# Performance work log

Measured on AMD Instinct MI355X. Metric: run time of the kernel, lower is better.

Reference implementation:

```python
import itertools
import jax
import jax.numpy as jnp
import numpy as np

FRAME_H, FRAME_W = 480, 640
HFOV = 79
CAM_H_CM = 88.0
NUM_SEM = 16
MAP_SIZE_CM, RES = 4800, 5
VR = 100
BEEN_CLOSE_CM = 200
GDS = 2
DU = 4
CAT_THR, EXP_THR, MAP_THR = 5.0, 1.0, 1.0
MIN_D_CM, MAX_D_CM = 50.0, 350.0
MIN_OBS_H_CM = 25
DIL_ITER, DIL_SIZE = 1, 3

NON_SEM = 4
LOCAL = MAP_SIZE_CM // GDS // RES
GLOBAL = MAP_SIZE_CM // RES
MAX_VH = int(360 / RES)
MIN_VH = int(-40 / RES)
ZB = MAX_VH - MIN_VH
MIN_Z = int(MIN_OBS_H_CM / RES - MIN_VH)
MAX_Z = int((CAM_H_CM + 1) / RES - MIN_VH)
XC = (FRAME_W - 1) / 2.0
ZC = (FRAME_H - 1) / 2.0
FOCAL = (FRAME_W / 2.0) / np.tan(np.deg2rad(HFOV / 2.0))
DEG = 57.29577951308232
B, T = 2, 4
C_MAP = NON_SEM + NUM_SEM

GPOSE0 = jnp.array([24.0, 24.0, 0.0], jnp.float32)
ORIG0 = jnp.array([12.0, 12.0, 0.0], jnp.float32)
LPOSE0 = GPOSE0 - ORIG0
LMB0 = jnp.array([240, 720, 240, 720], jnp.int32)

_XS = np.arange(FRAME_W, dtype=np.float32)[::DU]
_ZS = np.arange(FRAME_H - 1, -1, -1, dtype=np.float32)[::DU]


def point_cloud(depth):
    d = depth[:, ::DU, ::DU]
    valid = (d > MIN_D_CM) & (d < MAX_D_CM)
    X = (_XS[None, None, :] - XC) * d / FOCAL
    Z = (_ZS[None, :, None] - ZC) * d / FOCAL
    pts = jnp.stack([X, d, Z], -1).reshape(d.shape[0], -1, 3)
    return pts, valid.reshape(d.shape[0], -1)


def avg_pool(x, k):
    b, c, h, w = x.shape
    return x.reshape(b, c, h // k, k, w // k, k).mean((3, 5))


def splat(feat, coords):
    bs, fc, n = feat.shape
    dims = (VR, VR, ZB)
    G = VR * VR * ZB
    pos = [coords[:, d] * dims[d] / 2.0 + dims[d] / 2.0 for d in range(3)]
    fl = [jnp.floor(p) for p in pos]
    out = jnp.zeros((fc, bs * G), feat.dtype)
    offs = (jnp.arange(bs) * G)[:, None]
    for corner in itertools.product((0.0, 1.0), repeat=3):
        idx = jnp.zeros_like(pos[0])
        w = jnp.ones_like(pos[0])
        for d in range(3):
            p = fl[d] + corner[d]
            safe = ((p > 0) & (p < dims[d])).astype(feat.dtype)
            w = w * (1.0 - jnp.abs(pos[d] - p)) * safe
            idx = idx * dims[d] + p * safe
        flat = (idx.astype(jnp.int32) + offs).reshape(-1)
        vals = (feat * w[:, None, :]).transpose(1, 0, 2).reshape(fc, -1)
        out = out.at[:, flat].add(vals)
    out = jnp.round(out)
    return out.reshape(fc, bs, VR, VR, ZB).transpose(1, 0, 2, 3, 4)


def affine_grid(theta, h, w):
    ys = jnp.linspace(-1.0, 1.0, h)
    xs = jnp.linspace(-1.0, 1.0, w)
    gy, gx = jnp.meshgrid(ys, xs, indexing="ij")
    base = jnp.stack([gx, gy, jnp.ones_like(gx)], -1)
    return jnp.einsum("bij,hwj->bhwi", theta, base)


def _sample_one(im, grid):
    c, h, w = im.shape
    x = (grid[..., 0] + 1.0) * (w - 1) / 2.0
    y = (grid[..., 1] + 1.0) * (h - 1) / 2.0
    x0 = jnp.floor(x)
    y0 = jnp.floor(y)
    out = jnp.zeros((c,) + x.shape, im.dtype)
    for dx, dy in ((0, 0), (1, 0), (0, 1), (1, 1)):
        xi = x0 + dx
        yi = y0 + dy
        wgt = (1.0 - jnp.abs(x - xi)) * (1.0 - jnp.abs(y - yi))
        ok = (xi >= 0) & (xi <= w - 1) & (yi >= 0) & (yi <= h - 1)
        xi_c = jnp.clip(xi, 0, w - 1).astype(jnp.int32)
        yi_c = jnp.clip(yi, 0, h - 1).astype(jnp.int32)
        out = out + im[:, yi_c, xi_c] * (wgt * ok)[None]
    return out


grid_sample = jax.vmap(_sample_one)


def get_new_pose(pose, rel):
    s = jnp.sin(pose[:, 2] / DEG)
    c = jnp.cos(pose[:, 2] / DEG)
    x = pose[:, 0] + rel[:, 0] * c - rel[:, 1] * s
    y = pose[:, 1] + rel[:, 0] * s + rel[:, 1] * c
    o = pose[:, 2] + rel[:, 2] * DEG
    o = jnp.fmod(o - 180.0, 360.0) + 180.0
    o = jnp.fmod(o + 180.0, 360.0) - 180.0
    return jnp.stack([x, y, o], 1)


def update_local(obs, pdelta, prev_map, prev_pose):
    bs = obs.shape[0]
    pts, valid = point_cloud(obs[:, 3])
    pts = pts.at[..., 2].add(CAM_H_CM)
    pts = pts.at[..., 0].add(VR * RES / 2.0)
    cx = (pts[..., 0] / RES - VR // 2) / VR * 2.0
    cy = (pts[..., 1] / RES - VR // 2) / VR * 2.0
    cz = (pts[..., 2] / RES - (MAX_VH + MIN_VH) // 2) / ZB * 2.0
    coords = jnp.stack([cx, cy, cz], 1)
    coords = jnp.where(valid[:, None, :], coords, 2.0)
    sem = avg_pool(obs[:, 4:], DU).reshape(bs, NUM_SEM, -1)
    feat = jnp.concatenate([jnp.ones_like(sem[:, :1]), sem], 1)
    vox = splat(feat, coords)
    agent_h = vox[..., MIN_Z:MAX_Z].sum(-1)
    all_h = vox.sum(-1)
    fp_map = jnp.clip(agent_h[:, :1] / MAP_THR, 0.0, 1.0)
    fp_exp = jnp.clip(all_h[:, :1] / EXP_THR, 0.0, 1.0)
    sem_pred = jnp.clip(agent_h[:, 1:] / CAT_THR, 0.0, 1.0)
    x1 = LOCAL // 2 - VR // 2
    y1 = LOCAL // 2
    av = jnp.zeros((bs, C_MAP, LOCAL, LOCAL), obs.dtype)
    av = av.at[:, 0:1, y1:y1 + VR, x1:x1 + VR].set(fp_map)
    av = av.at[:, 1:2, y1:y1 + VR, x1:x1 + VR].set(fp_exp)
    av = av.at[:, NON_SEM:, y1:y1 + VR, x1:x1 + VR].set(sem_pred)
    pose = get_new_pose(prev_pose, pdelta)
    half = LOCAL // 2
    stx = -(pose[:, 0] * 100.0 / RES - half) / half
    sty = -(pose[:, 1] * 100.0 / RES - half) / half
    th = (90.0 - pose[:, 2]) * (np.pi / 180.0)
    ct, snt = jnp.cos(th), jnp.sin(th)
    zr, on = jnp.zeros_like(ct), jnp.ones_like(ct)
    th1 = jnp.stack([jnp.stack([ct, -snt, zr], -1), jnp.stack([snt, ct, zr], -1)], 1)
    th2 = jnp.stack([jnp.stack([on, zr, stx], -1), jnp.stack([zr, on, sty], -1)], 1)
    rotated = grid_sample(av, affine_grid(th1, LOCAL, LOCAL))
    translated = grid_sample(rotated, affine_grid(th2, LOCAL, LOCAL))
    cur = jnp.maximum(prev_map, translated)
    obst = cur[:, 0:1]
    kern = jnp.ones((1, 1, DIL_SIZE, DIL_SIZE), cur.dtype)
    for _ in range(DIL_ITER):
        obst = (jax.lax.conv(obst, kern, (1, 1), "SAME") > 0.5).astype(cur.dtype)
    cur = cur.at[:, 0].set(obst[:, 0])
    xg = (pose[:, 0] * 100.0 / RES).astype(jnp.int32)
    yg = (pose[:, 1] * 100.0 / RES).astype(jnp.int32)
    rr = jnp.arange(LOCAL)
    drow = rr[None, :, None] - yg[:, None, None]
    dcol = rr[None, None, :] - xg[:, None, None]
    sq = ((jnp.abs(drow) <= 2) & (jnp.abs(dcol) <= 2)).astype(cur.dtype)
    cur = cur.at[:, 2].set(sq)
    rad = BEEN_CLOSE_CM // RES
    disk = ((drow * drow + dcol * dcol) <= rad * rad).astype(cur.dtype)
    cur = cur.at[:, 3].set(jnp.maximum(cur[:, 3], disk))
    return cur, pose


def update_global_env(lmap, gmap, lpose, gpose, lmb, orig, updg):
    gpose_n = lpose + orig
    gmap_n = jax.lax.dynamic_update_slice(gmap, lmap, (0, lmb[0], lmb[2]))
    r = (gpose_n[1] * 100.0 / RES).astype(jnp.int32)
    c = (gpose_n[0] * 100.0 / RES).astype(jnp.int32)
    gx1 = jnp.clip(r - LOCAL // 2, 0, GLOBAL - LOCAL)
    gy1 = jnp.clip(c - LOCAL // 2, 0, GLOBAL - LOCAL)
    lmb_n = jnp.stack([gx1, gx1 + LOCAL, gy1, gy1 + LOCAL]).astype(jnp.int32)
    orig_n = jnp.stack([gy1 * RES / 100.0, gx1 * RES / 100.0, jnp.zeros(())]).astype(orig.dtype)
    lmap_n = jax.lax.dynamic_slice(gmap_n, (0, lmb_n[0], lmb_n[2]), lmap.shape)
    lpose_n = gpose_n - orig_n
    w = lambda a, b: jnp.where(updg, a, b)
    return (w(lmap_n, lmap), w(gmap_n, gmap), w(lpose_n, lpose),
            w(gpose_n, gpose), w(lmb_n, lmb), w(orig_n, orig))


def map_features(lmap, gmap):
    bs = gmap.shape[0]
    gdown = gmap[:, :NON_SEM].reshape(bs, NON_SEM, LOCAL, GDS, LOCAL, GDS).max((3, 5))
    return jnp.concatenate([lmap[:, :NON_SEM], gdown, lmap[:, NON_SEM:]], 1)


def forward(seq_obs, seq_pose_delta, seq_dones, seq_update_global, seq_camera_poses,
            init_local_map, init_global_map, init_local_pose, init_global_pose,
            init_lmb, init_origins):
    def step(carry, xs):
        lmap, gmap, lpose, gpose, lmb, orig = carry
        obs, pdelta, done, updg = xs
        d4 = done[:, None, None, None]
        d2 = done[:, None]
        lmap = jnp.where(d4, 0.0, lmap)
        gmap = jnp.where(d4, 0.0, gmap)
        lpose = jnp.where(d2, LPOSE0, lpose)
        gpose = jnp.where(d2, GPOSE0, gpose)
        lmb = jnp.where(d2, LMB0, lmb)
        orig = jnp.where(d2, ORIG0, orig)
        lmap, lpose = update_local(obs, pdelta, lmap, lpose)
        lmap, gmap, lpose, gpose, lmb, orig = jax.vmap(update_global_env)(
            lmap, gmap, lpose, gpose, lmb, orig, updg)
        feats = map_features(lmap, gmap)
        return (lmap, gmap, lpose, gpose, lmb, orig), (feats, lpose, gpose, lmb, orig)

    carry0 = (init_local_map, init_global_map, init_local_pose, init_global_pose,
              init_lmb, init_origins)
    xs = (jnp.swapaxes(seq_obs, 0, 1), jnp.swapaxes(seq_pose_delta, 0, 1),
          jnp.swapaxes(seq_dones, 0, 1), jnp.swapaxes(seq_update_global, 0, 1))
    (lmap, gmap, _, _, _, _), (fe, lp, gp, lb, og) = jax.lax.scan(step, carry0, xs)
    sw = lambda a: jnp.swapaxes(a, 0, 1)
    return sw(fe), lmap, gmap, sw(lp), sw(gp), sw(lb), sw(og)


def setup_inputs() -> dict:
    key = jax.random.key(0)
    ks = jax.random.split(key, 4)
    rgb = jax.random.uniform(ks[0], (B, T, 3, FRAME_H, FRAME_W), jnp.float32)
    depth = MIN_D_CM + jax.random.uniform(ks[1], (B, T, 1, FRAME_H, FRAME_W), jnp.float32) * (MAX_D_CM - MIN_D_CM + 100.0)
    seg = (jax.random.uniform(ks[2], (B, T, NUM_SEM, FRAME_H, FRAME_W)) > 0.95).astype(jnp.float32)
    seq_obs = jnp.concatenate([rgb, depth, seg], 2)
    seq_pose_delta = jax.random.normal(ks[3], (B, T, 3), jnp.float32) * jnp.array([0.25, 0.05, 0.1], jnp.float32)
    return {
        "seq_obs": seq_obs,
        "seq_pose_delta": seq_pose_delta,
        "seq_dones": jnp.zeros((B, T), bool),
        "seq_update_global": jnp.ones((B, T), bool),
        "seq_camera_poses": jnp.tile(jnp.eye(4, dtype=jnp.float32)[None], (B, 1, 1)),
        "init_local_map": jnp.zeros((B, C_MAP, LOCAL, LOCAL), jnp.float32),
        "init_global_map": jnp.zeros((B, C_MAP, GLOBAL, GLOBAL), jnp.float32),
        "init_local_pose": jnp.tile(LPOSE0[None], (B, 1)),
        "init_global_pose": jnp.tile(GPOSE0[None], (B, 1)),
        "init_lmb": jnp.tile(LMB0[None], (B, 1)),
        "init_origins": jnp.tile(ORIG0[None], (B, 1)),
    }


def reference(seq_obs, seq_pose_delta, seq_dones, seq_update_global, seq_camera_poses,
              init_local_map, init_global_map, init_local_pose, init_global_pose,
              init_lmb, init_origins):
    return forward(seq_obs, seq_pose_delta, seq_dones, seq_update_global, seq_camera_poses,
                   init_local_map, init_global_map, init_local_pose, init_global_pose,
                   init_lmb, init_origins)
```

## Files before the change

kernel.cpp:

```cpp
#include <hip/hip_runtime.h>
#include <math.h>


#define BB 2
#define TT 4
#define CMAP 20
#define LOC 480
#define GLOB 960
#define VOXC 17
#define NH 120
#define NW 160
#define NPTS (NH*NW)
#define LOC2 (LOC*LOC)
#define G2 (GLOB*GLOB)
#define FH 480
#define FW 640
#define LOCW 240
#define LOCW2 (LOCW*LOCW)
#define WOFF 120
#define CH0Z 69
#define SEMZ 12
#define CELLS 6100
#define CHSZ ((CH0Z + 16*SEMZ)*CELLS)

#define FE_OFF 0L
#define LM_OFF 44236800L
#define LM_SZ  9216000L
#define GM_OFF 53452800L
#define GM_SZ  36864000L
#define LP_OFF 90316800L
#define GP_OFF 90316824L
#define LB_OFF 90316848L
#define OG_OFF 90316880L

#define VOX_SZ   (2L*CHSZ)
#define RED_OFF  3184200L
#define ROT_OFF  3544200L
#define TMP_OFF  5617800L
#define CUR_OFF  6078600L
#define PTF_OFF  15294600L
#define PTI_OFF  15294664L
#define GLIN_OFF 15294728L

__device__ __forceinline__ int iabs(int v){ return v<0? -v : v; }

__global__ __launch_bounds__(256) void k_init0(float4* __restrict__ vox,
                                               float4* __restrict__ lmap,
                                               float4* __restrict__ gmap){
    const long NV4 = VOX_SZ/4;
    const long L4  = LM_SZ/4;
    const long G4  = GM_SZ/4;
    const long total = NV4+L4+G4;
    float4 z; z.x=0.f;z.y=0.f;z.z=0.f;z.w=0.f;
    long i = (long)blockIdx.x*blockDim.x + threadIdx.x;
    long st = (long)gridDim.x*blockDim.x;
    for(long k=i;k<total;k+=st){
        if(k<NV4) vox[k]=z;
        else if(k<NV4+L4) lmap[k-NV4]=z;
        else gmap[k-NV4-L4]=z;
    }
}

__global__ void k_poses(const float* __restrict__ ilp,const float* __restrict__ igp,
                        const int* __restrict__ ilmb,const float* __restrict__ iog,
                        const unsigned char* __restrict__ dones_raw,
                        const unsigned char* __restrict__ updg_raw,
                        const float* __restrict__ pdelta,
                        float* __restrict__ out,float* __restrict__ ptf,int* __restrict__ pti,
                        float* __restrict__ glin){
    #pragma clang fp contract(off)
    int tid = threadIdx.x;
    if(tid < LOC){
        float g;
        if(tid==LOC-1) g = 1.0f;
        else { float s = (float)tid/479.0f; g = s - (1.0f - s); }
        glin[tid] = g;
    }
    if(tid!=0 || blockIdx.x!=0) return;
    int stride;
    if(updg_raw[1]|updg_raw[2]|updg_raw[3]) stride = 1;
    else if(updg_raw[4])                    stride = 4;
    else                                    stride = 8;
    const float DEGF = 57.29577951308232f;
    for(int b=0;b<BB;b++){
        float lp0=ilp[b*3],lp1=ilp[b*3+1],lp2=ilp[b*3+2];
        float gp0=igp[b*3],gp1=igp[b*3+1],gp2=igp[b*3+2];
        float og0=iog[b*3],og1=iog[b*3+1],og2=iog[b*3+2];
        int m0=ilmb[b*4],m1=ilmb[b*4+1],m2=ilmb[b*4+2],m3=ilmb[b*4+3];
        for(int t=0;t<TT;t++){
            int dn = dones_raw[(b*TT+t)*stride]!=0;
            int ug = updg_raw[(b*TT+t)*stride]!=0;
            if(dn){
                lp0=12.f;lp1=12.f;lp2=0.f; gp0=24.f;gp1=24.f;gp2=0.f;
                og0=12.f;og1=12.f;og2=0.f; m0=240;m1=720;m2=240;m3=720;
            }
            float r0=pdelta[(b*TT+t)*3+0], r1=pdelta[(b*TT+t)*3+1], r2=pdelta[(b*TT+t)*3+2];
            float s=sinf(lp2/DEGF), c=cosf(lp2/DEGF);
            float x = lp0 + r0*c - r1*s;
            float y = lp1 + r0*s + r1*c;
            float o = lp2 + r2*DEGF;
            o = fmodf(o-180.f,360.f)+180.f;
            o = fmodf(o+180.f,360.f)-180.f;
            lp0=x; lp1=y; lp2=o;
            float th = (90.0f - o) * (float)(M_PI/180.0);
            float ct = cosf(th), snt = sinf(th);
            float ax = (lp0*100.0f)/5.0f;
            float ay = (lp1*100.0f)/5.0f;
            float stx = -((ax-240.0f)/240.0f);
            float sty = -((ay-240.0f)/240.0f);
            float* pf = ptf + (size_t)(t*BB+b)*8;
            pf[0]=lp0; pf[1]=lp1; pf[2]=o; pf[3]=ct; pf[4]=snt; pf[5]=stx; pf[6]=sty;
            int* pi = pti + (size_t)(t*BB+b)*8;
            pi[0]=m0; pi[1]=m2;
            pi[4]=(int)ax; pi[5]=(int)ay;
            pi[6]=dn; pi[7]=ug;
            float g0=lp0+og0, g1=lp1+og1, g2=lp2+og2;
            if(ug){
                int r  = (int)((g1*100.0f)/5.0f);
                int cc = (int)((g0*100.0f)/5.0f);
                int gx1 = min(max(r-240,0),480);
                int gy1 = min(max(cc-240,0),480);
                m0=gx1; m1=gx1+480; m2=gy1; m3=gy1+480;
                float o0 = ((float)gy1*5.0f)/100.0f;
                float o1 = ((float)gx1*5.0f)/100.0f;
                og0=o0; og1=o1; og2=0.f;
                lp0=g0-o0; lp1=g1-o1; lp2=g2;
                gp0=g0; gp1=g1; gp2=g2;
            }
            pi[2]=m0; pi[3]=m2;
            out[LP_OFF+(b*TT+t)*3+0]=lp0; out[LP_OFF+(b*TT+t)*3+1]=lp1; out[LP_OFF+(b*TT+t)*3+2]=lp2;
            out[GP_OFF+(b*TT+t)*3+0]=gp0; out[GP_OFF+(b*TT+t)*3+1]=gp1; out[GP_OFF+(b*TT+t)*3+2]=gp2;
            out[OG_OFF+(b*TT+t)*3+0]=og0; out[OG_OFF+(b*TT+t)*3+1]=og1; out[OG_OFF+(b*TT+t)*3+2]=og2;
            out[LB_OFF+(b*TT+t)*4+0]=(float)m0; out[LB_OFF+(b*TT+t)*4+1]=(float)m1;
            out[LB_OFF+(b*TT+t)*4+2]=(float)m2; out[LB_OFF+(b*TT+t)*4+3]=(float)m3;
        }
    }
}

__global__ __launch_bounds__(256) void k_reset_done(float4* __restrict__ lmap,float4* __restrict__ gmap,
                                                    const int* __restrict__ pti,int t){
    const long L4 = (long)CMAP*LOC2/4, G4 = (long)CMAP*G2/4, per = L4+G4;
    bool d0 = pti[(size_t)(t*BB+0)*8+6]!=0, d1 = pti[(size_t)(t*BB+1)*8+6]!=0;
    long total = (d0?per:0)+(d1?per:0);
    if(total==0) return;
    float4 z; z.x=0.f;z.y=0.f;z.z=0.f;z.w=0.f;
    long i = (long)blockIdx.x*blockDim.x + threadIdx.x;
    long st = (long)gridDim.x*blockDim.x;
    for(long k=i;k<total;k+=st){
        long r = k; int b;
        if(d0){ if(r<per) b=0; else { b=1; r-=per; } } else b=1;
        if(r<L4) lmap[b*L4+r]=z; else gmap[b*G4+(r-L4)]=z;
    }
}

__global__ __launch_bounds__(256) void k_splat(const float* __restrict__ obs,int t,
                                               float* __restrict__ vox,float FOCAL){
    #pragma clang fp contract(off)
    int tid = blockIdx.x*blockDim.x + threadIdx.x;
    if(tid >= BB*VOXC*NPTS) return;
    int p  = tid % NPTS;
    int ch = (tid/NPTS) % VOXC;
    int b  = tid / (VOXC*NPTS);
    int zi = p / NW, xi = p % NW;
    const float* ob = obs + ((size_t)(b*TT+t))*CMAP*FH*FW;
    float d = ob[3*FH*FW + (size_t)(4*zi)*FW + 4*xi];
    if(!(d>50.0f && d<350.0f)) return;
    float f;
    if(ch==0) f = 1.0f;
    else{
        const float* cp = ob + (size_t)(4+ch-1)*FH*FW + (size_t)(4*zi)*FW + 4*xi;
        float s=0.f;
        #pragma unroll
        for(int r=0;r<4;r++){
            float4 v = *(const float4*)(cp + (size_t)r*FW);
            s += v.x+v.y+v.z+v.w;
        }
        f = s*0.0625f;
    }
    float X  = ((float)(4*xi) - 319.5f)*d/FOCAL;
    float Zc = ((float)(479-4*zi) - 239.5f)*d/FOCAL;
    float p0f = X + 250.0f;
    float p1f = d;
    float p2f = Zc + 88.0f;
    float cx = (p0f/5.0f - 50.0f)/100.0f*2.0f;
    float cy = (p1f/5.0f - 50.0f)/100.0f*2.0f;
    float cz = (p2f/5.0f - 32.0f)/80.0f*2.0f;
    float pos0 = cx*100.0f/2.0f + 50.0f;
    float pos1 = cy*100.0f/2.0f + 50.0f;
    float pos2 = cz*80.0f/2.0f + 40.0f;
    float f0=floorf(pos0), f1=floorf(pos1), f2=floorf(pos2);
    float* base = vox + (size_t)b*CHSZ;
    #pragma unroll
    for(int c0=0;c0<2;c0++){
        float q0=f0+(float)c0;
        if(!(q0>0.f && q0<100.f)) continue;
        float w0 = 1.0f-fabsf(pos0-q0);
        int iq0 = (int)q0;
        #pragma unroll
        for(int c1=0;c1<2;c1++){
            float q1=f1+(float)c1;
            if(!(q1>=10.0f && q1<=70.0f)) continue;
            float w1 = w0*(1.0f-fabsf(pos1-q1));
            int cell = iq0*61 + ((int)q1-10);
            #pragma unroll
            for(int c2=0;c2<2;c2++){
                float q2=f2+(float)c2;
                if(!(q2>0.f && q2<70.f)) continue;
                int iq2 = (int)q2;
                float w = w1*(1.0f-fabsf(pos2-q2));
                if(ch==0)
                    atomicAdd(base + (size_t)(iq2-1)*CELLS + cell, w);
                else if(iq2>=13 && iq2<25)
                    atomicAdd(base + (size_t)(CH0Z + (ch-1)*SEMZ + (iq2-13))*CELLS + cell, f*w);
            }
        }
    }
}

__global__ __launch_bounds__(256) void k_reduce(float* __restrict__ vox,float* __restrict__ red){
    int tid = blockIdx.x*blockDim.x + threadIdx.x;
    if(tid >= BB*VOXC*10000) return;
    int cell = tid % 10000;
    int ch   = (tid/10000) % VOXC;
    int b    = tid / (VOXC*10000);
    int q0 = cell/100, q1 = cell%100;
    float allh=0.f, ag=0.f;
    if(q1>=10 && q1<=70){
        float* base = vox + (size_t)b*CHSZ;
        if(ch==0){
            float* vp = base + q0*61 + (q1-10);
            for(int z=0;z<CH0Z;z++){
                float v = rintf(vp[(size_t)z*CELLS]);
                allh += v;
                if(z>=12 && z<24) ag += v;
                vp[(size_t)z*CELLS] = 0.0f;
            }
        }else{
            float* vp = base + (size_t)(CH0Z + (ch-1)*SEMZ)*CELLS + q0*61 + (q1-10);
            for(int z=0;z<SEMZ;z++){
                float v = rintf(vp[(size_t)z*CELLS]);
                ag += v;
                vp[(size_t)z*CELLS] = 0.0f;
            }
        }
    }
    float* rb = red + (size_t)b*18*10000;
    if(ch==0){
        rb[cell]       = fminf(fmaxf(ag,0.f),1.f);
        rb[10000+cell] = fminf(fmaxf(allh,0.f),1.f);
    }else{
        rb[(ch+1)*10000+cell] = fminf(fmaxf(ag/5.0f,0.f),1.f);
    }
}

__global__ __launch_bounds__(256) void k_rot(const float* __restrict__ red,const float* __restrict__ ptf,
                                             const float* __restrict__ glin,int t,
                                             float* __restrict__ rotW){
    #pragma clang fp contract(off)
    int tid = blockIdx.x*blockDim.x + threadIdx.x;
    if(tid >= BB*LOCW2) return;
    int wx = tid % LOCW;
    int wy = (tid/LOCW) % LOCW;
    int b  = tid / LOCW2;
    int x = wx + WOFF, y = wy + WOFF;
    const float* pf = ptf + (size_t)(t*BB+b)*8;
    float ct = pf[3], snt = pf[4];
    float gx = glin[x], gy = glin[y];
    float grx = ct*gx - snt*gy;
    float gry = snt*gx + ct*gy;
    float xs = (grx+1.0f)*239.5f;
    float ys = (gry+1.0f)*239.5f;
    float x0 = floorf(xs), y0 = floorf(ys);
    int   off[4]; float w[4];
    #pragma unroll
    for(int k=0;k<4;k++){
        float xi = x0 + (float)(k&1), yi = y0 + (float)(k>>1);
        float wgt = (1.0f-fabsf(xs-xi))*(1.0f-fabsf(ys-yi));
        int xii=(int)xi, yii=(int)yi;
        bool ok = !(xi<0.f||xi>479.f||yi<0.f||yi>479.f)
                  && yii>=240 && yii<340 && xii>=190 && xii<290;
        w[k]   = ok ? wgt : 0.0f;
        off[k] = ok ? (yii-240)*100 + (xii-190) : 0;
    }
    const float* rb = red + (size_t)b*18*10000;
    float* rp = rotW + (size_t)b*18*LOCW2 + (size_t)wy*LOCW + wx;
    for(int ch=0;ch<18;ch++){
        const float* rc = rb + (size_t)ch*10000;
        float acc = rc[off[0]]*w[0];
        acc += rc[off[1]]*w[1];
        acc += rc[off[2]]*w[2];
        acc += rc[off[3]]*w[3];
        rp[(size_t)ch*LOCW2] = acc;
    }
}

__global__ __launch_bounds__(256) void k_trans(const float* __restrict__ rotW,const float* __restrict__ ptf,
                                               const int* __restrict__ pti,const float* __restrict__ glin,
                                               int t,const float* __restrict__ P,
                                               float* __restrict__ C,float* __restrict__ tmp0){
    #pragma clang fp contract(off)
    int tid = blockIdx.x*blockDim.x + threadIdx.x;
    if(tid >= BB*LOC2) return;
    int x = tid % LOC;
    int y = (tid/LOC) % LOC;
    int b = tid / LOC2;
    const float* pf = ptf + (size_t)(t*BB+b)*8;
    const int*   pi = pti + (size_t)(t*BB+b)*8;
    float stx = pf[5], sty = pf[6];
    float xs = (glin[x]+stx+1.0f)*239.5f;
    float ys = (glin[y]+sty+1.0f)*239.5f;
    float x0=floorf(xs), y0=floorf(ys);
    int   off[4]; float w[4];
    #pragma unroll
    for(int k=0;k<4;k++){
        float xi = x0 + (float)(k&1), yi = y0 + (float)(k>>1);
        float wgt = (1.0f-fabsf(xs-xi))*(1.0f-fabsf(ys-yi));
        int xii=(int)xi, yii=(int)yi;
        bool ok = !(xi<0.f||xi>479.f||yi<0.f||yi>479.f)
                  && xii>=WOFF && xii<WOFF+LOCW && yii>=WOFF && yii<WOFF+LOCW;
        w[k]   = ok ? wgt : 0.0f;
        off[k] = ok ? (yii-WOFF)*LOCW + (xii-WOFF) : 0;
    }
    int xg=pi[4], yg=pi[5];
    float sq   = (iabs(y-yg)<=2 && iabs(x-xg)<=2) ? 1.0f : 0.0f;
    int dr=y-yg, dc=x-xg;
    float disk = (dr*dr+dc*dc <= 1600) ? 1.0f : 0.0f;
    const float* rb = rotW + (size_t)b*18*LOCW2;
    size_t pix = (size_t)y*LOC + x;
    const float* Pb = P + (size_t)b*CMAP*LOC2 + pix;
    float* Cb = C + (size_t)b*CMAP*LOC2 + pix;
    for(int c=0;c<CMAP;c++){
        if(c==2){ Cb[2*LOC2] = sq; continue; }
        if(c==3){ Cb[3*LOC2] = fmaxf(Pb[3*LOC2], disk); continue; }
        int wc = (c<2) ? c : c-2;
        const float* rp = rb + (size_t)wc*LOCW2;
        float acc = rp[off[0]]*w[0];
        acc += rp[off[1]]*w[1];
        acc += rp[off[2]]*w[2];
        acc += rp[off[3]]*w[3];
        float res = fmaxf(Pb[(size_t)c*LOC2], acc);
        if(c==0) tmp0[(size_t)b*LOC2 + pix] = res;
        else     Cb[(size_t)c*LOC2] = res;
    }
}

__global__ __launch_bounds__(256) void k_dil(const float* __restrict__ tmp0,float* __restrict__ C){
    int tid = blockIdx.x*blockDim.x + threadIdx.x;
    if(tid >= BB*LOC2) return;
    int x = tid % LOC;
    int y = (tid/LOC) % LOC;
    int b = tid / LOC2;
    const float* tb = tmp0 + (size_t)b*LOC2;
    float s=0.f;
    for(int dy=-1;dy<=1;dy++){
        int yy=y+dy; if(yy<0||yy>=LOC) continue;
        for(int dx=-1;dx<=1;dx++){
            int xx=x+dx; if(xx<0||xx>=LOC) continue;
            s += tb[(size_t)yy*LOC+xx];
        }
    }
    C[(size_t)b*CMAP*LOC2 + (size_t)y*LOC + x] = (s>0.5f)?1.0f:0.0f;
}

__global__ __launch_bounds__(256) void k_out(const float* __restrict__ C,float* __restrict__ gmap,
                                             float* __restrict__ P,float* __restrict__ fe,
                                             const int* __restrict__ pti,int t){
    int tid = blockIdx.x*blockDim.x + threadIdx.x;
    if(tid >= BB*LOC2) return;
    int x = tid % LOC;
    int y = (tid/LOC) % LOC;
    int b = tid / LOC2;
    const int* pi = pti + (size_t)(t*BB+b)*8;
    int r0o=pi[0], c0o=pi[1], r0n=pi[2], c0n=pi[3];
    int ug = pi[7];
    size_t pix = (size_t)y*LOC + x;
    const float* Cb = C + (size_t)b*CMAP*LOC2;
    float* gB = gmap + (size_t)b*CMAP*G2;
    float* pB = P + (size_t)b*CMAP*LOC2;
    float* feB = fe + ((size_t)(b*TT+t))*24*LOC2;
    if(ug){
        size_t gp = (size_t)(r0o+y)*GLOB + (c0o+x);
        for(int c=0;c<CMAP;c++)
            gB[(size_t)c*G2 + gp] = Cb[(size_t)c*LOC2 + pix];
    }
    int dr = ug ? (r0n - r0o) : 0;
    int dc = ug ? (c0n - c0o) : 0;
    int sy = y + dr, sx = x + dc;
    bool inT = (sy>=0 && sy<LOC && sx>=0 && sx<LOC);
    size_t gpn = ug ? ((size_t)(r0n+y)*GLOB + (c0n+x)) : 0;
    size_t spix = (size_t)sy*LOC + sx;
    for(int c=0;c<CMAP;c++){
        float v = inT ? Cb[(size_t)c*LOC2 + spix]
                      : gB[(size_t)c*G2 + gpn];
        pB[(size_t)c*LOC2 + pix] = v;
        int fc = (c<4) ? c : c+4;
        feB[(size_t)fc*LOC2 + pix] = v;
    }
    for(int gc=0;gc<4;gc++){
        float m = 0.f; bool first = true;
        #pragma unroll
        for(int dy=0;dy<2;dy++){
            #pragma unroll
            for(int dx=0;dx<2;dx++){
                int ty = 2*y+dy, tx = 2*x+dx;
                int ly = ty - r0o, lx = tx - c0o;
                float tv;
                if(ug && ly>=0 && ly<LOC && lx>=0 && lx<LOC)
                    tv = Cb[(size_t)gc*LOC2 + (size_t)ly*LOC + lx];
                else
                    tv = gB[(size_t)gc*G2 + (size_t)ty*GLOB + tx];
                m = first ? tv : fmaxf(m, tv);
                first = false;
            }
        }
        feB[(size_t)(4+gc)*LOC2 + pix] = m;
    }
}

extern "C" void kernel_launch(void* const* d_in, const int* in_sizes, int n_in,
                              void* d_out, int out_size, void* d_ws, size_t ws_size,
                              hipStream_t stream){
    const float* obs    = (const float*)d_in[0];
    const float* pdelta = (const float*)d_in[1];
    const unsigned char* dones_raw = (const unsigned char*)d_in[2];
    const unsigned char* updg_raw  = (const unsigned char*)d_in[3];
    const float* ilp  = (const float*)d_in[7];
    const float* igp  = (const float*)d_in[8];
    const int*   ilmb = (const int*)d_in[9];
    const float* iog  = (const float*)d_in[10];

    float* out  = (float*)d_out;
    float* fe   = out + FE_OFF;
    float* lmap = out + LM_OFF;
    float* gmap = out + GM_OFF;

    float* ws   = (float*)d_ws;
    float* vox  = ws;
    float* red  = ws + RED_OFF;
    float* rotW = ws + ROT_OFF;
    float* tmp0 = ws + TMP_OFF;
    float* curm = ws + CUR_OFF;
    float* ptf  = ws + PTF_OFF;
    int*   pti  = (int*)(ws + PTI_OFF);
    float* glin = ws + GLIN_OFF;

    const float FOCAL = (float)(320.0 / tan(39.5 * M_PI / 180.0));

    k_init0<<<2048,256,0,stream>>>((float4*)vox,(float4*)lmap,(float4*)gmap);
    k_poses<<<1,512,0,stream>>>(ilp,igp,ilmb,iog,dones_raw,updg_raw,pdelta,out,ptf,pti,glin);

    for(int t=0;t<TT;t++){
        k_reset_done<<<2048,256,0,stream>>>((float4*)lmap,(float4*)gmap,pti,t);
        { int n=BB*VOXC*NPTS;   k_splat <<<(n+255)/256,256,0,stream>>>(obs,t,vox,FOCAL); }
        { int n=BB*VOXC*10000;  k_reduce<<<(n+255)/256,256,0,stream>>>(vox,red); }
        { int n=BB*LOCW2;       k_rot   <<<(n+255)/256,256,0,stream>>>(red,ptf,glin,t,rotW); }
        { int n=BB*LOC2;        k_trans <<<(n+255)/256,256,0,stream>>>(rotW,ptf,pti,glin,t,lmap,curm,tmp0); }
        { int n=BB*LOC2;        k_dil   <<<(n+255)/256,256,0,stream>>>(tmp0,curm); }
        { int n=BB*LOC2;        k_out   <<<(n+255)/256,256,0,stream>>>(curm,gmap,lmap,fe,pti,t); }
    }
}
```

Baseline: 1.093 ms.

## Fuse all pipeline stages into one cooperative persistent kernel with grid syncs

Replaces the sequence of about thirty separate kernel launches (init, poses, then per-timestep reset, splat, reduce, rotate, translate, dilate and output) with a single cooperative kernel. It uses grid-stride loops over each stage and grid.sync() between dependent stages. Stage bodies are factored into device functions shared with the old kernels, which remain as a fallback if the cooperative launch fails. This removes per-launch overhead and inter-kernel gaps. In exchange it fixes the grid at 1024 blocks of 256 threads under a stricter launch bound, which may raise register pressure and lower occupancy, and each grid-wide barrier has its own cost.

```diff
diff --git a/kernel.cpp b/kernel.cpp
--- a/kernel.cpp
+++ b/kernel.cpp
@@ -1,5 +1,8 @@
 #include <hip/hip_runtime.h>
+#include <hip/hip_cooperative_groups.h>
 #include <math.h>
+
+namespace cg = cooperative_groups;
 
 
 #define BB 2
@@ -44,39 +47,21 @@
 
 __device__ __forceinline__ int iabs(int v){ return v<0? -v : v; }
 
-__global__ __launch_bounds__(256) void k_init0(float4* __restrict__ vox,
-                                               float4* __restrict__ lmap,
-                                               float4* __restrict__ gmap){
-    const long NV4 = VOX_SZ/4;
-    const long L4  = LM_SZ/4;
-    const long G4  = GM_SZ/4;
-    const long total = NV4+L4+G4;
-    float4 z; z.x=0.f;z.y=0.f;z.z=0.f;z.w=0.f;
-    long i = (long)blockIdx.x*blockDim.x + threadIdx.x;
-    long st = (long)gridDim.x*blockDim.x;
-    for(long k=i;k<total;k+=st){
-        if(k<NV4) vox[k]=z;
-        else if(k<NV4+L4) lmap[k-NV4]=z;
-        else gmap[k-NV4-L4]=z;
-    }
-}
-
-__global__ void k_poses(const float* __restrict__ ilp,const float* __restrict__ igp,
-                        const int* __restrict__ ilmb,const float* __restrict__ iog,
-                        const unsigned char* __restrict__ dones_raw,
-                        const unsigned char* __restrict__ updg_raw,
-                        const float* __restrict__ pdelta,
-                        float* __restrict__ out,float* __restrict__ ptf,int* __restrict__ pti,
-                        float* __restrict__ glin){
+
+__device__ __forceinline__ void glin_body(int i, float* glin){
+    float g;
+    if(i==LOC-1) g = 1.0f;
+    else { float s = (float)i/479.0f; g = s - (1.0f - s); }
+    glin[i] = g;
+}
+
+__device__ void poses_body(const float* ilp,const float* igp,
+                           const int* ilmb,const float* iog,
+                           const unsigned char* dones_raw,
+                           const unsigned char* updg_raw,
+                           const float* pdelta,
+                           float* out,float* ptf,int* pti){
     #pragma clang fp contract(off)
-    int tid = threadIdx.x;
-    if(tid < LOC){
-        float g;
-        if(tid==LOC-1) g = 1.0f;
-        else { float s = (float)tid/479.0f; g = s - (1.0f - s); }
-        glin[tid] = g;
-    }
-    if(tid!=0 || blockIdx.x!=0) return;
     int stride;
     if(updg_raw[1]|updg_raw[2]|updg_raw[3]) stride = 1;
     else if(updg_raw[4])                    stride = 4;
@@ -137,27 +122,9 @@
     }
 }
 
-__global__ __launch_bounds__(256) void k_reset_done(float4* __restrict__ lmap,float4* __restrict__ gmap,
-                                                    const int* __restrict__ pti,int t){
-    const long L4 = (long)CMAP*LOC2/4, G4 = (long)CMAP*G2/4, per = L4+G4;
-    bool d0 = pti[(size_t)(t*BB+0)*8+6]!=0, d1 = pti[(size_t)(t*BB+1)*8+6]!=0;
-    long total = (d0?per:0)+(d1?per:0);
-    if(total==0) return;
-    float4 z; z.x=0.f;z.y=0.f;z.z=0.f;z.w=0.f;
-    long i = (long)blockIdx.x*blockDim.x + threadIdx.x;
-    long st = (long)gridDim.x*blockDim.x;
-    for(long k=i;k<total;k+=st){
-        long r = k; int b;
-        if(d0){ if(r<per) b=0; else { b=1; r-=per; } } else b=1;
-        if(r<L4) lmap[b*L4+r]=z; else gmap[b*G4+(r-L4)]=z;
-    }
-}
-
-__global__ __launch_bounds__(256) void k_splat(const float* __restrict__ obs,int t,
-                                               float* __restrict__ vox,float FOCAL){
+__device__ __forceinline__ void splat_body(int tid,const float* __restrict__ obs,int t,
+                                           float* __restrict__ vox,float FOCAL){
     #pragma clang fp contract(off)
-    int tid = blockIdx.x*blockDim.x + threadIdx.x;
-    if(tid >= BB*VOXC*NPTS) return;
     int p  = tid % NPTS;
     int ch = (tid/NPTS) % VOXC;
     int b  = tid / (VOXC*NPTS);
@@ -217,9 +184,7 @@
     }
 }
 
-__global__ __launch_bounds__(256) void k_reduce(float* __restrict__ vox,float* __restrict__ red){
-    int tid = blockIdx.x*blockDim.x + threadIdx.x;
-    if(tid >= BB*VOXC*10000) return;
+__device__ __forceinline__ void reduce_body(int tid,float* __restrict__ vox,float* __restrict__ red){
     int cell = tid % 10000;
     int ch   = (tid/10000) % VOXC;
     int b    = tid / (VOXC*10000);
@@ -253,12 +218,11 @@
     }
 }
 
-__global__ __launch_bounds__(256) void k_rot(const float* __restrict__ red,const float* __restrict__ ptf,
-                                             const float* __restrict__ glin,int t,
-                                             float* __restrict__ rotW){
+__device__ __forceinline__ void rot_body(int tid,const float* __restrict__ red,
+                                         const float* __restrict__ ptf,
+                                         const float* __restrict__ glin,int t,
+                                         float* __restrict__ rotW){
     #pragma clang fp contract(off)
-    int tid = blockIdx.x*blockDim.x + threadIdx.x;
-    if(tid >= BB*LOCW2) return;
     int wx = tid % LOCW;
     int wy = (tid/LOCW) % LOCW;
     int b  = tid / LOCW2;
@@ -294,13 +258,12 @@
     }
 }
 
-__global__ __launch_bounds__(256) void k_trans(const float* __restrict__ rotW,const float* __restrict__ ptf,
-                                               const int* __restrict__ pti,const float* __restrict__ glin,
-                                               int t,const float* __restrict__ P,
-                                               float* __restrict__ C,float* __restrict__ tmp0){
+__device__ __forceinline__ void trans_body(int tid,const float* __restrict__ rotW,
+                                           const float* __restrict__ ptf,const int* __restrict__ pti,
+                                           const float* __restrict__ glin,int t,
+                                           const float* __restrict__ P,
+                                           float* __restrict__ C,float* __restrict__ tmp0){
     #pragma clang fp contract(off)
-    int tid = blockIdx.x*blockDim.x + threadIdx.x;
-    if(tid >= BB*LOC2) return;
     int x = tid % LOC;
     int y = (tid/LOC) % LOC;
     int b = tid / LOC2;
@@ -344,9 +307,7 @@
     }
 }
 
-__global__ __launch_bounds__(256) void k_dil(const float* __restrict__ tmp0,float* __restrict__ C){
-    int tid = blockIdx.x*blockDim.x + threadIdx.x;
-    if(tid >= BB*LOC2) return;
+__device__ __forceinline__ void dil_body(int tid,const float* __restrict__ tmp0,float* __restrict__ C){
     int x = tid % LOC;
     int y = (tid/LOC) % LOC;
     int b = tid / LOC2;
@@ -362,11 +323,9 @@
     C[(size_t)b*CMAP*LOC2 + (size_t)y*LOC + x] = (s>0.5f)?1.0f:0.0f;
 }
 
-__global__ __launch_bounds__(256) void k_out(const float* __restrict__ C,float* __restrict__ gmap,
-                                             float* __restrict__ P,float* __restrict__ fe,
-                                             const int* __restrict__ pti,int t){
-    int tid = blockIdx.x*blockDim.x + threadIdx.x;
-    if(tid >= BB*LOC2) return;
+__device__ __forceinline__ void out_body(int tid,const float* __restrict__ C,float* __restrict__ gmap,
+                                         float* __restrict__ P,float* __restrict__ fe,
+                                         const int* __restrict__ pti,int t){
     int x = tid % LOC;
     int y = (tid/LOC) % LOC;
     int b = tid / LOC2;
@@ -417,6 +376,156 @@
     }
 }
 
+__global__ __launch_bounds__(256,4) void k_mega(
+        const float* __restrict__ obs,const float* __restrict__ pdelta,
+        const unsigned char* __restrict__ dones_raw,const unsigned char* __restrict__ updg_raw,
+        const float* __restrict__ ilp,const float* __restrict__ igp,
+        const int* __restrict__ ilmb,const float* __restrict__ iog,
+        float* __restrict__ out,float* __restrict__ ws,float FOCAL){
+    cg::grid_group grid = cg::this_grid();
+    const int NT = (int)(gridDim.x*blockDim.x);
+    const int gt = (int)(blockIdx.x*blockDim.x + threadIdx.x);
+
+    float* fe   = out + FE_OFF;
+    float* lmap = out + LM_OFF;
+    float* gmap = out + GM_OFF;
+    float* vox  = ws;
+    float* red  = ws + RED_OFF;
+    float* rotW = ws + ROT_OFF;
+    float* tmp0 = ws + TMP_OFF;
+    float* curm = ws + CUR_OFF;
+    float* ptf  = ws + PTF_OFF;
+    int*   pti  = (int*)(ws + PTI_OFF);
+    float* glin = ws + GLIN_OFF;
+
+    if(gt < LOC) glin_body(gt, glin);
+    if(gt == 0) poses_body(ilp,igp,ilmb,iog,dones_raw,updg_raw,pdelta,out,ptf,pti);
+    {
+        float4* v4=(float4*)vox; float4* l4=(float4*)lmap; float4* g4=(float4*)gmap;
+        const long NV4=VOX_SZ/4, L4=LM_SZ/4, G4=GM_SZ/4, total=NV4+L4+G4;
+        float4 z; z.x=0.f;z.y=0.f;z.z=0.f;z.w=0.f;
+        for(long k=gt;k<total;k+=NT){
+            if(k<NV4) v4[k]=z;
+            else if(k<NV4+L4) l4[k-NV4]=z;
+            else g4[k-NV4-L4]=z;
+        }
+    }
+    grid.sync();
+
+    for(int t=0;t<TT;t++){
+        {
+            const long L4=(long)CMAP*LOC2/4, G4=(long)CMAP*G2/4, per=L4+G4;
+            bool d0 = pti[(size_t)(t*BB+0)*8+6]!=0, d1 = pti[(size_t)(t*BB+1)*8+6]!=0;
+            long totalr = (d0?per:0)+(d1?per:0);
+            if(totalr){
+                float4* l4=(float4*)lmap; float4* g4=(float4*)gmap;
+                float4 z; z.x=0.f;z.y=0.f;z.z=0.f;z.w=0.f;
+                for(long k=gt;k<totalr;k+=NT){
+                    long r=k; int b;
+                    if(d0){ if(r<per) b=0; else { b=1; r-=per; } } else b=1;
+                    if(r<L4) l4[b*L4+r]=z; else g4[b*G4+(r-L4)]=z;
+                }
+            }
+            for(int i=gt;i<BB*VOXC*NPTS;i+=NT) splat_body(i,obs,t,vox,FOCAL);
+        }
+        grid.sync();
+        for(int i=gt;i<BB*VOXC*10000;i+=NT) reduce_body(i,vox,red);
+        grid.sync();
+        for(int i=gt;i<BB*LOCW2;i+=NT) rot_body(i,red,ptf,glin,t,rotW);
+        grid.sync();
+        for(int i=gt;i<BB*LOC2;i+=NT) trans_body(i,rotW,ptf,pti,glin,t,lmap,curm,tmp0);
+        grid.sync();
+        for(int i=gt;i<BB*LOC2;i+=NT) dil_body(i,tmp0,curm);
+        grid.sync();
+        for(int i=gt;i<BB*LOC2;i+=NT) out_body(i,curm,gmap,lmap,fe,pti,t);
+        grid.sync();
+    }
+}
+
+__global__ __launch_bounds__(256) void k_init0(float4* __restrict__ vox,
+                                               float4* __restrict__ lmap,
+                                               float4* __restrict__ gmap){
+    const long NV4 = VOX_SZ/4, L4 = LM_SZ/4, G4 = GM_SZ/4;
+    const long total = NV4+L4+G4;
+    float4 z; z.x=0.f;z.y=0.f;z.z=0.f;z.w=0.f;
+    long i = (long)blockIdx.x*blockDim.x + threadIdx.x;
+    long st = (long)gridDim.x*blockDim.x;
+    for(long k=i;k<total;k+=st){
+        if(k<NV4) vox[k]=z;
+        else if(k<NV4+L4) lmap[k-NV4]=z;
+        else gmap[k-NV4-L4]=z;
+    }
+}
+
+__global__ void k_poses(const float* ilp,const float* igp,const int* ilmb,const float* iog,
+                        const unsigned char* dones_raw,const unsigned char* updg_raw,
+                        const float* pdelta,float* out,float* ptf,int* pti,float* glin){
+    int tid = threadIdx.x;
+    if(tid < LOC) glin_body(tid, glin);
+    if(tid!=0 || blockIdx.x!=0) return;
+    poses_body(ilp,igp,ilmb,iog,dones_raw,updg_raw,pdelta,out,ptf,pti);
+}
+
+__global__ __launch_bounds__(256) void k_reset_done(float4* __restrict__ lmap,float4* __restrict__ gmap,
+                                                    const int* __restrict__ pti,int t){
+    const long L4 = (long)CMAP*LOC2/4, G4 = (long)CMAP*G2/4, per = L4+G4;
+    bool d0 = pti[(size_t)(t*BB+0)*8+6]!=0, d1 = pti[(size_t)(t*BB+1)*8+6]!=0;
+    long total = (d0?per:0)+(d1?per:0);
+    if(total==0) return;
+    float4 z; z.x=0.f;z.y=0.f;z.z=0.f;z.w=0.f;
+    long i = (long)blockIdx.x*blockDim.x + threadIdx.x;
+    long st = (long)gridDim.x*blockDim.x;
+    for(long k=i;k<total;k+=st){
+        long r = k; int b;
+        if(d0){ if(r<per) b=0; else { b=1; r-=per; } } else b=1;
+        if(r<L4) lmap[b*L4+r]=z; else gmap[b*G4+(r-L4)]=z;
+    }
+}
+
+__global__ __launch_bounds__(256) void k_splat(const float* __restrict__ obs,int t,
+                                               float* __restrict__ vox,float FOCAL){
+    int tid = blockIdx.x*blockDim.x + threadIdx.x;
+    if(tid >= BB*VOXC*NPTS) return;
+    splat_body(tid,obs,t,vox,FOCAL);
+}
+
+__global__ __launch_bounds__(256) void k_reduce(float* __restrict__ vox,float* __restrict__ red){
+    int tid = blockIdx.x*blockDim.x + threadIdx.x;
+    if(tid >= BB*VOXC*10000) return;
+    reduce_body(tid,vox,red);
+}
+
+__global__ __launch_bounds__(256) void k_rot(const float* __restrict__ red,const float* __restrict__ ptf,
+                                             const float* __restrict__ glin,int t,
+                                             float* __restrict__ rotW){
+    int tid = blockIdx.x*blockDim.x + threadIdx.x;
+    if(tid >= BB*LOCW2) return;
+    rot_body(tid,red,ptf,glin,t,rotW);
+}
+
+__global__ __launch_bounds__(256) void k_trans(const float* __restrict__ rotW,const float* __restrict__ ptf,
+                                               const int* __restrict__ pti,const float* __restrict__ glin,
+                                               int t,const float* __restrict__ P,
+                                               float* __restrict__ C,float* __restrict__ tmp0){
+    int tid = blockIdx.x*blockDim.x + threadIdx.x;
+    if(tid >= BB*LOC2) return;
+    trans_body(tid,rotW,ptf,pti,glin,t,P,C,tmp0);
+}
+
+__global__ __launch_bounds__(256) void k_dil(const float* __restrict__ tmp0,float* __restrict__ C){
+    int tid = blockIdx.x*blockDim.x + threadIdx.x;
+    if(tid >= BB*LOC2) return;
+    dil_body(tid,tmp0,C);
+}
+
+__global__ __launch_bounds__(256) void k_out(const float* __restrict__ C,float* __restrict__ gmap,
+                                             float* __restrict__ P,float* __restrict__ fe,
+                                             const int* __restrict__ pti,int t){
+    int tid = blockIdx.x*blockDim.x + threadIdx.x;
+    if(tid >= BB*LOC2) return;
+    out_body(tid,C,gmap,P,fe,pti,t);
+}
+
 extern "C" void kernel_launch(void* const* d_in, const int* in_sizes, int n_in,
                               void* d_out, int out_size, void* d_ws, size_t ws_size,
                               hipStream_t stream){
@@ -430,25 +539,31 @@
     const float* iog  = (const float*)d_in[10];
 
     float* out  = (float*)d_out;
+    float* wsf  = (float*)d_ws;
+    const float FOCAL = (float)(320.0 / tan(39.5 * M_PI / 180.0));
+
+    void* args[] = { (void*)&obs, (void*)&pdelta, (void*)&dones_raw, (void*)&updg_raw,
+                     (void*)&ilp, (void*)&igp, (void*)&ilmb, (void*)&iog,
+                     (void*)&out, (void*)&wsf, (void*)&FOCAL };
+    hipError_t cerr = hipLaunchCooperativeKernel((void*)k_mega,
+                                                 dim3(1024), dim3(256),
+                                                 args, 0, stream);
+    if(cerr == hipSuccess) return;
+
     float* fe   = out + FE_OFF;
     float* lmap = out + LM_OFF;
     float* gmap = out + GM_OFF;
-
-    float* ws   = (float*)d_ws;
-    float* vox  = ws;
-    float* red  = ws + RED_OFF;
-    float* rotW = ws + ROT_OFF;
-    float* tmp0 = ws + TMP_OFF;
-    float* curm = ws + CUR_OFF;
-    float* ptf  = ws + PTF_OFF;
-    int*   pti  = (int*)(ws + PTI_OFF);
-    float* glin = ws + GLIN_OFF;
-
-    const float FOCAL = (float)(320.0 / tan(39.5 * M_PI / 180.0));
+    float* vox  = wsf;
+    float* red  = wsf + RED_OFF;
+    float* rotW = wsf + ROT_OFF;
+    float* tmp0 = wsf + TMP_OFF;
+    float* curm = wsf + CUR_OFF;
+    float* ptf  = wsf + PTF_OFF;
+    int*   pti  = (int*)(wsf + PTI_OFF);
+    float* glin = wsf + GLIN_OFF;
 
     k_init0<<<2048,256,0,stream>>>((float4*)vox,(float4*)lmap,(float4*)gmap);
     k_poses<<<1,512,0,stream>>>(ilp,igp,ilmb,iog,dones_raw,updg_raw,pdelta,out,ptf,pti,glin);
-
     for(int t=0;t<TT;t++){
         k_reset_done<<<2048,256,0,stream>>>((float4*)lmap,(float4*)gmap,pti,t);
         { int n=BB*VOXC*NPTS;   k_splat <<<(n+255)/256,256,0,stream>>>(obs,t,vox,FOCAL); }
```

New measurement: 4.261 ms. +289.9%, slower.
